# Performance work log

Hardware: AMD Instinct MI355X
Metric: run time of the kernel (lower is better)

The kernel has to match this reference:

```python
import jax, jax.numpy as jnp
import numpy as np

K_NEIGHBORS = 8   # num_neighbors init arg
BETA = 0.5        # smooth-L1 beta
EPS = 1e-8        # torch cosine_similarity eps


def setup_inputs() -> dict:
    key = jax.random.key(0)
    k1, k2, k3 = jax.random.split(key, 3)
    B, N, D, C = 16, 1024, 768, 2
    return {
        "student_emb": jax.random.normal(k1, (B, N, D), dtype=jnp.float32),
        "teacher_emb": jax.random.normal(k2, (B, N, D), dtype=jnp.float32),
        "centers": jax.random.normal(k3, (B, N, C), dtype=jnp.float32),
    }


def _cosine(anchor, nb):
    # anchor [B,N,1,D], nb [B,N,K,D] -> [B,N,K]
    dot = jnp.sum(anchor * nb, axis=-1)
    na = jnp.maximum(jnp.linalg.norm(anchor, axis=-1), EPS)
    nb_n = jnp.maximum(jnp.linalg.norm(nb, axis=-1), EPS)
    return dot / (na * nb_n)


def reference(student_emb, teacher_emb, centers):
    B, N, _ = centers.shape
    k = min(K_NEIGHBORS + 1, N)
    # brute-force pairwise squared distances [B,N,N] (knn_points)
    sq = jnp.sum(centers * centers, axis=-1)
    d2 = sq[:, :, None] + sq[:, None, :] - 2.0 * jnp.einsum("bnc,bmc->bnm", centers, centers)
    _, idx = jax.lax.top_k(-d2, k)   # ascending distance; idx [B,N,k]
    idx = idx[:, :, 1:]               # drop self (distance 0 is first)
    # knn_gather: neighbors [B,N,K,D]
    gather = jax.vmap(lambda e, i: e[i])
    student_nb = gather(student_emb, idx)
    teacher_nb = gather(teacher_emb, idx)
    student_rel = _cosine(student_emb[:, :, None, :], student_nb)  # [B,N,K]
    teacher_rel = jax.lax.stop_gradient(_cosine(teacher_emb[:, :, None, :], teacher_nb))
    diff = jnp.abs(student_rel - teacher_rel)
    sl1 = jnp.where(diff < BETA, 0.5 * diff * diff / BETA, diff - 0.5 * BETA)
    per_patch = sl1.mean(axis=-1)  # [B,N]
    return per_patch.mean()        # reduction='mean'
```

## Files before the change

kernel.cpp:

```cpp
#include <hip/hip_runtime.h>
#include <hip/hip_fp16.h>
#include <math.h>

#define BB 16
#define NN 1024
#define DD 768
#define KK 8
#define BETA_F 0.5f
#define EPS_F 1e-8f

#define TPK_BLOCKS ((BB * NN) / 4)
#define NORM_BLOCKS ((BB * NN) / 4)

typedef _Float16 h2_t __attribute__((ext_vector_type(2)));

#if defined(__has_builtin)
#if __has_builtin(__builtin_amdgcn_fdot2)
#define HAVE_FDOT2 1
#endif
#endif

__device__ __forceinline__ float dot4acc(uint2 a, uint2 b, float acc) {
#ifdef HAVE_FDOT2
    acc = __builtin_amdgcn_fdot2(__builtin_bit_cast(h2_t, a.x),
                                 __builtin_bit_cast(h2_t, b.x), acc, false);
    acc = __builtin_amdgcn_fdot2(__builtin_bit_cast(h2_t, a.y),
                                 __builtin_bit_cast(h2_t, b.y), acc, false);
#else
    float2 fa = __half22float2(__builtin_bit_cast(__half2, a.x));
    float2 fb = __half22float2(__builtin_bit_cast(__half2, b.x));
    acc = fmaf(fa.x, fb.x, acc); acc = fmaf(fa.y, fb.y, acc);
    fa = __half22float2(__builtin_bit_cast(__half2, a.y));
    fb = __half22float2(__builtin_bit_cast(__half2, b.y));
    acc = fmaf(fa.x, fb.x, acc); acc = fmaf(fa.y, fb.y, acc);
#endif
    return acc;
}

__device__ __forceinline__ double wave_min_f64_to_all(double x) {
#define DPPMIN(CTRL, RM) {                                                  \
        uint2 u_ = __builtin_bit_cast(uint2, x);                            \
        uint2 y_;                                                           \
        y_.x = (unsigned)__builtin_amdgcn_update_dpp((int)u_.x, (int)u_.x,  \
                                                     CTRL, RM, 0xf, false); \
        y_.y = (unsigned)__builtin_amdgcn_update_dpp((int)u_.y, (int)u_.y,  \
                                                     CTRL, RM, 0xf, false); \
        x = fmin(x, __builtin_bit_cast(double, y_));                        \
    }
    DPPMIN(0x111, 0xf)
    DPPMIN(0x112, 0xf)
    DPPMIN(0x114, 0xf)
    DPPMIN(0x118, 0xf)
    DPPMIN(0x142, 0xa)
    DPPMIN(0x143, 0xc)
#undef DPPMIN
    uint2 u = __builtin_bit_cast(uint2, x);
    uint2 r;
    r.x = (unsigned)__builtin_amdgcn_readlane((int)u.x, 63);
    r.y = (unsigned)__builtin_amdgcn_readlane((int)u.y, 63);
    return __builtin_bit_cast(double, r);
}

__device__ __forceinline__ unsigned topk_u(float anx, float any_, float sqn, float4 c) {
    float dot = anx * c.x + any_ * c.y;
    float d2  = (sqn + c.z) - 2.0f * dot;
    unsigned int u = __float_as_uint(d2);
    u ^= (unsigned int)((int)u >> 31) | 0x80000000u;
    return u;
}

#define KINF 1.0e300

#define K16(X) X(0) X(1) X(2) X(3) X(4) X(5) X(6) X(7) \
               X(8) X(9) X(10) X(11) X(12) X(13) X(14) X(15)

#define MINTREE() fmin(fmin(fmin(fmin(k0,k1),fmin(k2,k3)),                 \
                            fmin(fmin(k4,k5),fmin(k6,k7))),               \
                       fmin(fmin(fmin(k8,k9),fmin(k10,k11)),              \
                            fmin(fmin(k12,k13),fmin(k14,k15))))

__device__ __forceinline__ void topk_wave_body(const float* __restrict__ centers,
                                               int* __restrict__ idx_out,
                                               int tb, int tid, float4* c4) {
    const int b    = tb >> 8;
    const int grp  = tb & 255;
    const int wave = tid >> 6;
    const int lane = tid & 63;

    const float4* cbase = (const float4*)(centers + (size_t)b * NN * 2);
    for (int i = tid; i < NN / 2; i += 256) {
        float4 v = cbase[i];
        c4[2 * i + 0] = make_float4(v.x, v.y, v.x * v.x + v.y * v.y, 0.f);
        c4[2 * i + 1] = make_float4(v.z, v.w, v.z * v.z + v.w * v.w, 0.f);
    }
    __syncthreads();

    const int    n   = grp * 4 + wave;
    const float4 cn  = c4[n];
    const float  anx = cn.x, any_ = cn.y, sqn = cn.z;

#define DK(i) double k##i;
    K16(DK)
#undef DK
#define IK(i) { const int m_ = (i) * 64 + lane;                            \
                float4 c_ = c4[m_];                                        \
                unsigned u_ = topk_u(anx, any_, sqn, c_);                  \
                k##i = fma((double)u_, 1024.0, (double)m_); }
    K16(IK)
#undef IK

    double lm = MINTREE();
    int mm[9];

#define VK(i) k##i = (k##i == g) ? KINF : k##i;
#define TOPK_ROUND(r) {                                                    \
        const double g = wave_min_f64_to_all(lm);                          \
        double qf = floor(g * 0.0009765625) * 1024.0;                      \
        mm[r] = (int)(g - qf);                                             \
        K16(VK)                                                            \
        lm = MINTREE();                                                    \
    }
    TOPK_ROUND(0)
    TOPK_ROUND(1)
    TOPK_ROUND(2)
    TOPK_ROUND(3)
    TOPK_ROUND(4)
    TOPK_ROUND(5)
    TOPK_ROUND(6)
    TOPK_ROUND(7)
    TOPK_ROUND(8)
#undef TOPK_ROUND
#undef VK

    if (lane == 0) {
        int* outp = idx_out + ((size_t)b * NN + n) * KK;
        ((int4*)outp)[0] = make_int4(mm[1], mm[2], mm[3], mm[4]);
        ((int4*)outp)[1] = make_int4(mm[5], mm[6], mm[7], mm[8]);
    }
}

__device__ __forceinline__ void normh_body(const float* __restrict__ s,
                                           const float* __restrict__ t,
                                           __half* __restrict__ ns,
                                           __half* __restrict__ nt,
                                           int nb, int tid) {
    const int row  = nb * 4 + (tid >> 6);
    const int lane = tid & 63;
    const float4* srow = (const float4*)(s + (size_t)row * DD);
    const float4* trow = (const float4*)(t + (size_t)row * DD);
    float4 vs[3], vt[3];
    float ss = 0.f, tt = 0.f;
#pragma unroll
    for (int i = 0; i < 3; ++i) {
        vs[i] = srow[lane + 64 * i];
        vt[i] = trow[lane + 64 * i];
        ss = fmaf(vs[i].x, vs[i].x, fmaf(vs[i].y, vs[i].y,
             fmaf(vs[i].z, vs[i].z, fmaf(vs[i].w, vs[i].w, ss))));
        tt = fmaf(vt[i].x, vt[i].x, fmaf(vt[i].y, vt[i].y,
             fmaf(vt[i].z, vt[i].z, fmaf(vt[i].w, vt[i].w, tt))));
    }
#pragma unroll
    for (int m = 1; m < 64; m <<= 1) {
        ss += __shfl_xor(ss, m);
        tt += __shfl_xor(tt, m);
    }
    const float is_ = 1.0f / fmaxf(sqrtf(ss), EPS_F);
    const float it_ = 1.0f / fmaxf(sqrtf(tt), EPS_F);

    uint2* nsrow = (uint2*)(ns + (size_t)row * DD);
    uint2* ntrow = (uint2*)(nt + (size_t)row * DD);
#pragma unroll
    for (int i = 0; i < 3; ++i) {
        __half2 a0 = __floats2half2_rn(vs[i].x * is_, vs[i].y * is_);
        __half2 a1 = __floats2half2_rn(vs[i].z * is_, vs[i].w * is_);
        __half2 b0 = __floats2half2_rn(vt[i].x * it_, vt[i].y * it_);
        __half2 b1 = __floats2half2_rn(vt[i].z * it_, vt[i].w * it_);
        uint2 ua; ua.x = __builtin_bit_cast(unsigned int, a0);
        ua.y = __builtin_bit_cast(unsigned int, a1);
        uint2 ub; ub.x = __builtin_bit_cast(unsigned int, b0);
        ub.y = __builtin_bit_cast(unsigned int, b1);
        nsrow[lane + 64 * i] = ua;
        ntrow[lane + 64 * i] = ub;
    }
}

__global__ __launch_bounds__(256, 4) void fused_prep(const float* __restrict__ centers,
                                                     const float* __restrict__ s,
                                                     const float* __restrict__ t,
                                                     int* __restrict__ idx_out,
                                                     __half* __restrict__ ns,
                                                     __half* __restrict__ nt) {
    __shared__ float4 c4[NN];
    const int role = blockIdx.x & 1;
    const int tb   = blockIdx.x >> 1;
    if (role == 0)
        topk_wave_body(centers, idx_out, tb, threadIdx.x, c4);
    else
        normh_body(s, t, ns, nt, tb, threadIdx.x);
}

__global__ __launch_bounds__(256, 4) void topk_kernel(const float* __restrict__ centers,
                                                      int* __restrict__ idx_out) {
    __shared__ float4 c4[NN];
    topk_wave_body(centers, idx_out, blockIdx.x, threadIdx.x, c4);
}

__global__ __launch_bounds__(256) void lossh_kernel(const __half* __restrict__ ns,
                                                    const __half* __restrict__ nt,
                                                    const int* __restrict__ idx,
                                                    float* __restrict__ part) {
    const int bid  = blockIdx.x;
    const int v    = (bid & 7) * 512 + (bid >> 3);
    const int wave = threadIdx.x >> 6;
    const int lane = threadIdx.x & 63;
    const int p    = v * 4 + wave;
    const int base = p & ~(NN - 1);

    int q[8];
    {
        const int4* ip = (const int4*)(idx + (size_t)p * KK);
        int4 a = ip[0], c = ip[1];
        q[0] = base + a.x; q[1] = base + a.y; q[2] = base + a.z; q[3] = base + a.w;
        q[4] = base + c.x; q[5] = base + c.y; q[6] = base + c.z; q[7] = base + c.w;
    }

    const uint2* srow = (const uint2*)(ns + (size_t)p * DD);
    const uint2* trow = (const uint2*)(nt + (size_t)p * DD);
    uint2 sa[3], ta[3];
#pragma unroll
    for (int c = 0; c < 3; ++c) {
        sa[c] = srow[lane + 64 * c];
        ta[c] = trow[lane + 64 * c];
    }

    uint2 sv[8][3], tv[8][3];
#pragma unroll
    for (int j = 0; j < 8; ++j) {
        const uint2* snb = (const uint2*)(ns + (size_t)q[j] * DD);
        const uint2* tnb = (const uint2*)(nt + (size_t)q[j] * DD);
#pragma unroll
        for (int c = 0; c < 3; ++c) {
            sv[j][c] = snb[lane + 64 * c];
            tv[j][c] = tnb[lane + 64 * c];
        }
    }

    float ds[8], dt[8];
#pragma unroll
    for (int j = 0; j < 8; ++j) {
        float a = 0.f, b = 0.f;
#pragma unroll
        for (int c = 0; c < 3; ++c) {
            a = dot4acc(sa[c], sv[j][c], a);
            b = dot4acc(ta[c], tv[j][c], b);
        }
        ds[j] = a;
        dt[j] = b;
    }
#pragma unroll
    for (int m = 1; m < 64; m <<= 1) {
#pragma unroll
        for (int j = 0; j < 8; ++j) {
            ds[j] += __shfl_xor(ds[j], m);
            dt[j] += __shfl_xor(dt[j], m);
        }
    }
    float sum = 0.f;
#pragma unroll
    for (int j = 0; j < 8; ++j) {
        const float diff = fabsf(ds[j] - dt[j]);
        sum += diff < BETA_F ? (0.5f * diff * diff / BETA_F) : (diff - 0.5f * BETA_F);
    }

    __shared__ float wpart[4];
    if (lane == 0) wpart[wave] = sum;
    __syncthreads();
    if (threadIdx.x == 0)
        part[v] = (wpart[0] + wpart[1]) + (wpart[2] + wpart[3]);
}

__global__ __launch_bounds__(256) void norm_kernel(const float* __restrict__ s,
                                                   const float* __restrict__ t,
                                                   float* __restrict__ inv_s,
                                                   float* __restrict__ inv_t) {
    const int row  = blockIdx.x * 4 + (threadIdx.x >> 6);
    const int lane = threadIdx.x & 63;
    const float4* srow = (const float4*)(s + (size_t)row * DD);
    const float4* trow = (const float4*)(t + (size_t)row * DD);
    float ss = 0.f, tt = 0.f;
#pragma unroll
    for (int i = 0; i < 3; ++i) {
        float4 v = srow[lane + 64 * i];
        ss = fmaf(v.x, v.x, fmaf(v.y, v.y, fmaf(v.z, v.z, fmaf(v.w, v.w, ss))));
        float4 w = trow[lane + 64 * i];
        tt = fmaf(w.x, w.x, fmaf(w.y, w.y, fmaf(w.z, w.z, fmaf(w.w, w.w, tt))));
    }
#pragma unroll
    for (int m = 1; m < 64; m <<= 1) {
        ss += __shfl_xor(ss, m);
        tt += __shfl_xor(tt, m);
    }
    if (lane == 0) {
        inv_s[row] = 1.0f / fmaxf(sqrtf(ss), EPS_F);
        inv_t[row] = 1.0f / fmaxf(sqrtf(tt), EPS_F);
    }
}

__global__ __launch_bounds__(256) void lossf_kernel(const float* __restrict__ s,
                                                    const float* __restrict__ t,
                                                    const int* __restrict__ idx,
                                                    const float* __restrict__ inv_s,
                                                    const float* __restrict__ inv_t,
                                                    float* __restrict__ part) {
    const int wave = threadIdx.x >> 6;
    const int lane = threadIdx.x & 63;
    const int p    = blockIdx.x * 4 + wave;
    const int base = p & ~(NN - 1);
    int q[8];
    {
        const int4* ip = (const int4*)(idx + (size_t)p * KK);
        int4 a = ip[0], c = ip[1];
        q[0] = base + a.x; q[1] = base + a.y; q[2] = base + a.z; q[3] = base + a.w;
        q[4] = base + c.x; q[5] = base + c.y; q[6] = base + c.z; q[7] = base + c.w;
    }
    float isq[8], itq[8];
#pragma unroll
    for (int j = 0; j < 8; ++j) { isq[j] = inv_s[q[j]]; itq[j] = inv_t[q[j]]; }
    const float isn = inv_s[p];
    const float itn = inv_t[p];
    const float4* srow = (const float4*)(s + (size_t)p * DD);
    const float4* trow = (const float4*)(t + (size_t)p * DD);
    float4 as0 = srow[lane], as1 = srow[lane + 64], as2 = srow[lane + 128];
    float4 at0 = trow[lane], at1 = trow[lane + 64], at2 = trow[lane + 128];
    float ds[8], dt[8];
#pragma unroll
    for (int j = 0; j < 8; ++j) {
        const float4* snb = (const float4*)(s + (size_t)q[j] * DD);
        const float4* tnb = (const float4*)(t + (size_t)q[j] * DD);
        float4 v0 = snb[lane], v1 = snb[lane + 64], v2 = snb[lane + 128];
        float4 w0 = tnb[lane], w1 = tnb[lane + 64], w2 = tnb[lane + 128];
        float a = 0.f, b = 0.f;
        a = fmaf(as0.x, v0.x, a); a = fmaf(as0.y, v0.y, a);
        a = fmaf(as0.z, v0.z, a); a = fmaf(as0.w, v0.w, a);
        a = fmaf(as1.x, v1.x, a); a = fmaf(as1.y, v1.y, a);
        a = fmaf(as1.z, v1.z, a); a = fmaf(as1.w, v1.w, a);
        a = fmaf(as2.x, v2.x, a); a = fmaf(as2.y, v2.y, a);
        a = fmaf(as2.z, v2.z, a); a = fmaf(as2.w, v2.w, a);
        b = fmaf(at0.x, w0.x, b); b = fmaf(at0.y, w0.y, b);
        b = fmaf(at0.z, w0.z, b); b = fmaf(at0.w, w0.w, b);
        b = fmaf(at1.x, w1.x, b); b = fmaf(at1.y, w1.y, b);
        b = fmaf(at1.z, w1.z, b); b = fmaf(at1.w, w1.w, b);
        b = fmaf(at2.x, w2.x, b); b = fmaf(at2.y, w2.y, b);
        b = fmaf(at2.z, w2.z, b); b = fmaf(at2.w, w2.w, b);
        ds[j] = a; dt[j] = b;
    }
#pragma unroll
    for (int m = 1; m < 64; m <<= 1) {
#pragma unroll
        for (int j = 0; j < 8; ++j) {
            ds[j] += __shfl_xor(ds[j], m);
            dt[j] += __shfl_xor(dt[j], m);
        }
    }
    float sum = 0.f;
#pragma unroll
    for (int j = 0; j < 8; ++j) {
        const float cs   = ds[j] * isn * isq[j];
        const float ct   = dt[j] * itn * itq[j];
        const float diff = fabsf(cs - ct);
        sum += diff < BETA_F ? (0.5f * diff * diff / BETA_F) : (diff - 0.5f * BETA_F);
    }
    __shared__ float wpart[4];
    if (lane == 0) wpart[wave] = sum;
    __syncthreads();
    if (threadIdx.x == 0)
        part[blockIdx.x] = (wpart[0] + wpart[1]) + (wpart[2] + wpart[3]);
}

__global__ __launch_bounds__(256) void finalize_kernel(const float* __restrict__ part,
                                                       float* __restrict__ out) {
    __shared__ float red[256];
    float acc = 0.f;
    for (int i = threadIdx.x; i < (BB * NN) / 4; i += 256) acc += part[i];
    red[threadIdx.x] = acc;
    __syncthreads();
    for (int off = 128; off > 0; off >>= 1) {
        if (threadIdx.x < off) red[threadIdx.x] += red[threadIdx.x + off];
        __syncthreads();
    }
    if (threadIdx.x == 0) out[0] = red[0] * (1.0f / (float)(BB * NN * KK));
}

extern "C" void kernel_launch(void* const* d_in, const int* in_sizes, int n_in,
                              void* d_out, int out_size, void* d_ws, size_t ws_size,
                              hipStream_t stream) {
    const float* student = (const float*)d_in[0];
    const float* teacher = (const float*)d_in[1];
    const float* centers = (const float*)d_in[2];
    float* out = (float*)d_out;

    const size_t idx_bytes  = (size_t)BB * NN * KK * sizeof(int);
    const size_t half_bytes = (size_t)BB * NN * DD * sizeof(__half);
    const size_t part_bytes = 4096 * sizeof(float);
    int* idx_buf = (int*)d_ws;

    if (ws_size >= idx_bytes + 2 * half_bytes + part_bytes) {
        __half* ns  = (__half*)((char*)d_ws + idx_bytes);
        __half* nt  = ns + (size_t)BB * NN * DD;
        float* part = (float*)((char*)d_ws + idx_bytes + 2 * half_bytes);
        fused_prep<<<TPK_BLOCKS + NORM_BLOCKS, 256, 0, stream>>>(centers, student,
                                                                 teacher, idx_buf, ns, nt);
        lossh_kernel<<<NORM_BLOCKS, 256, 0, stream>>>(ns, nt, idx_buf, part);
        finalize_kernel<<<1, 256, 0, stream>>>(part, out);
    } else {
        float* inv_s = (float*)((char*)d_ws + idx_bytes);
        float* inv_t = inv_s + BB * NN;
        float* part  = inv_t + BB * NN;
        topk_kernel<<<TPK_BLOCKS, 256, 0, stream>>>(centers, idx_buf);
        norm_kernel<<<NORM_BLOCKS, 256, 0, stream>>>(student, teacher, inv_s, inv_t);
        lossf_kernel<<<NORM_BLOCKS, 256, 0, stream>>>(student, teacher, idx_buf,
                                                      inv_s, inv_t, part);
        finalize_kernel<<<1, 256, 0, stream>>>(part, out);
    }
}
```

Baseline: 93.73 us.

## Process two query points per wave in top-k and rebalance fused prep blocks

Each top-k wave now selects neighbors for two points at once, interleaving two independent wave-min reduction chains so their latency can overlap. The number of top-k blocks is halved, and the fused prep kernel interleaves one top-k block with two normalization blocks. Inline asm pins the keys in VGPRs, and launch bounds drop the min-blocks hint. This doubles per-thread register use for keys (32 doubles), which may lower occupancy.

After: 84.66 us. -9.7%, faster.

```diff
diff --git a/kernel.cpp b/kernel.cpp
--- a/kernel.cpp
+++ b/kernel.cpp
@@ -9,7 +9,7 @@
 #define BETA_F 0.5f
 #define EPS_F 1e-8f
 
-#define TPK_BLOCKS ((BB * NN) / 4)
+#define TPK_BLOCKS ((BB * NN) / 8)
 #define NORM_BLOCKS ((BB * NN) / 4)
 
 typedef _Float16 h2_t __attribute__((ext_vector_type(2)));
@@ -71,19 +71,47 @@
 
 #define KINF 1.0e300
 
-#define K16(X) X(0) X(1) X(2) X(3) X(4) X(5) X(6) X(7) \
-               X(8) X(9) X(10) X(11) X(12) X(13) X(14) X(15)
-
-#define MINTREE() fmin(fmin(fmin(fmin(k0,k1),fmin(k2,k3)),                 \
-                            fmin(fmin(k4,k5),fmin(k6,k7))),               \
-                       fmin(fmin(fmin(k8,k9),fmin(k10,k11)),              \
-                            fmin(fmin(k12,k13),fmin(k14,k15))))
+struct Keys { double k[16]; };
+
+#define PIN_KEYS(K)                                                         \
+    asm("" : "+v"(K.k[0]),  "+v"(K.k[1]),  "+v"(K.k[2]),  "+v"(K.k[3]),    \
+             "+v"(K.k[4]),  "+v"(K.k[5]),  "+v"(K.k[6]),  "+v"(K.k[7]),    \
+             "+v"(K.k[8]),  "+v"(K.k[9]),  "+v"(K.k[10]), "+v"(K.k[11]),   \
+             "+v"(K.k[12]), "+v"(K.k[13]), "+v"(K.k[14]), "+v"(K.k[15]))
+
+__device__ __forceinline__ void initkeys(Keys& K, float anx, float any_, float sqn,
+                                         const float4* c4, int lane) {
+#pragma unroll
+    for (int i = 0; i < 16; ++i) {
+        const int m_ = i * 64 + lane;
+        float4 c_ = c4[m_];
+        unsigned u_ = topk_u(anx, any_, sqn, c_);
+        K.k[i] = fma((double)u_, 1024.0, (double)m_);
+    }
+}
+
+__device__ __forceinline__ double mintree(const Keys& K) {
+    return fmin(fmin(fmin(fmin(K.k[0], K.k[1]),  fmin(K.k[2], K.k[3])),
+                     fmin(fmin(K.k[4], K.k[5]),  fmin(K.k[6], K.k[7]))),
+                fmin(fmin(fmin(K.k[8], K.k[9]),  fmin(K.k[10], K.k[11])),
+                     fmin(fmin(K.k[12], K.k[13]), fmin(K.k[14], K.k[15]))));
+}
+
+__device__ __forceinline__ void killkey(Keys& K, double g) {
+#pragma unroll
+    for (int i = 0; i < 16; ++i) K.k[i] = (K.k[i] == g) ? KINF : K.k[i];
+}
+
+__device__ __forceinline__ int decode_m(double g) {
+    double qf = floor(g * 0.0009765625) * 1024.0;
+    return (int)(g - qf);
+}
 
 __device__ __forceinline__ void topk_wave_body(const float* __restrict__ centers,
                                                int* __restrict__ idx_out,
                                                int tb, int tid, float4* c4) {
-    const int b    = tb >> 8;
-    const int grp  = tb & 255;
+    const int b    = tb >> 7;
+    const int grp  = tb & 127;
     const int wave = tid >> 6;
     const int lane = tid & 63;
 
@@ -95,47 +123,41 @@
     }
     __syncthreads();
 
-    const int    n   = grp * 4 + wave;
-    const float4 cn  = c4[n];
-    const float  anx = cn.x, any_ = cn.y, sqn = cn.z;
-
-#define DK(i) double k##i;
-    K16(DK)
-#undef DK
-#define IK(i) { const int m_ = (i) * 64 + lane;                            \
-                float4 c_ = c4[m_];                                        \
-                unsigned u_ = topk_u(anx, any_, sqn, c_);                  \
-                k##i = fma((double)u_, 1024.0, (double)m_); }
-    K16(IK)
-#undef IK
-
-    double lm = MINTREE();
-    int mm[9];
-
-#define VK(i) k##i = (k##i == g) ? KINF : k##i;
-#define TOPK_ROUND(r) {                                                    \
-        const double g = wave_min_f64_to_all(lm);                          \
-        double qf = floor(g * 0.0009765625) * 1024.0;                      \
-        mm[r] = (int)(g - qf);                                             \
-        K16(VK)                                                            \
-        lm = MINTREE();                                                    \
-    }
-    TOPK_ROUND(0)
-    TOPK_ROUND(1)
-    TOPK_ROUND(2)
-    TOPK_ROUND(3)
-    TOPK_ROUND(4)
-    TOPK_ROUND(5)
-    TOPK_ROUND(6)
-    TOPK_ROUND(7)
-    TOPK_ROUND(8)
-#undef TOPK_ROUND
-#undef VK
+    const int nA = grp * 8 + wave * 2;
+    const int nB = nA + 1;
+    const float4 cA = c4[nA];
+    const float4 cB = c4[nB];
+
+    Keys KA, KB;
+    initkeys(KA, cA.x, cA.y, cA.z, c4, lane);
+    initkeys(KB, cB.x, cB.y, cB.z, c4, lane);
+    PIN_KEYS(KA);
+    PIN_KEYS(KB);
+
+    double lmA = mintree(KA);
+    double lmB = mintree(KB);
+    int mmA[9], mmB[9];
+
+#pragma unroll
+    for (int r = 0; r < 9; ++r) {
+        const double gA = wave_min_f64_to_all(lmA);
+        const double gB = wave_min_f64_to_all(lmB);
+        mmA[r] = decode_m(gA);
+        mmB[r] = decode_m(gB);
+        killkey(KA, gA);
+        killkey(KB, gB);
+        PIN_KEYS(KA);
+        PIN_KEYS(KB);
+        lmA = mintree(KA);
+        lmB = mintree(KB);
+    }
 
     if (lane == 0) {
-        int* outp = idx_out + ((size_t)b * NN + n) * KK;
-        ((int4*)outp)[0] = make_int4(mm[1], mm[2], mm[3], mm[4]);
-        ((int4*)outp)[1] = make_int4(mm[5], mm[6], mm[7], mm[8]);
+        int* outp = idx_out + ((size_t)b * NN + nA) * KK;
+        ((int4*)outp)[0] = make_int4(mmA[1], mmA[2], mmA[3], mmA[4]);
+        ((int4*)outp)[1] = make_int4(mmA[5], mmA[6], mmA[7], mmA[8]);
+        ((int4*)outp)[2] = make_int4(mmB[1], mmB[2], mmB[3], mmB[4]);
+        ((int4*)outp)[3] = make_int4(mmB[5], mmB[6], mmB[7], mmB[8]);
     }
 }
 
@@ -184,23 +206,23 @@
     }
 }
 
-__global__ __launch_bounds__(256, 4) void fused_prep(const float* __restrict__ centers,
-                                                     const float* __restrict__ s,
-                                                     const float* __restrict__ t,
-                                                     int* __restrict__ idx_out,
-                                                     __half* __restrict__ ns,
-                                                     __half* __restrict__ nt) {
+__global__ __launch_bounds__(256) void fused_prep(const float* __restrict__ centers,
+                                                  const float* __restrict__ s,
+                                                  const float* __restrict__ t,
+                                                  int* __restrict__ idx_out,
+                                                  __half* __restrict__ ns,
+                                                  __half* __restrict__ nt) {
     __shared__ float4 c4[NN];
-    const int role = blockIdx.x & 1;
-    const int tb   = blockIdx.x >> 1;
-    if (role == 0)
-        topk_wave_body(centers, idx_out, tb, threadIdx.x, c4);
+    const int r3 = blockIdx.x % 3;
+    const int q3 = blockIdx.x / 3;
+    if (r3 == 0)
+        topk_wave_body(centers, idx_out, q3, threadIdx.x, c4);
     else
-        normh_body(s, t, ns, nt, tb, threadIdx.x);
-}
-
-__global__ __launch_bounds__(256, 4) void topk_kernel(const float* __restrict__ centers,
-                                                      int* __restrict__ idx_out) {
+        normh_body(s, t, ns, nt, q3 * 2 + (r3 - 1), threadIdx.x);
+}
+
+__global__ __launch_bounds__(256) void topk_kernel(const float* __restrict__ centers,
+                                                   int* __restrict__ idx_out) {
     __shared__ float4 c4[NN];
     topk_wave_body(centers, idx_out, blockIdx.x, threadIdx.x, c4);
 }
```
